# Kernel tuning notes

Measured on AMD Instinct MI355X. Metric: run time of the kernel, lower is better.

Reference implementation:

```python
import jax, jax.numpy as jnp
import numpy as np

B, T, M, C, H = 2, 2048, 2048, 1024, 16
D = C // H  # head_size = 64


def setup_inputs() -> dict:
    key = jax.random.key(0)
    ks = jax.random.split(key, 8)
    s = 0.02
    return {
        "relative_positions": jax.random.normal(ks[0], (H, T, T + M), jnp.float32),
        "x": jax.random.normal(ks[1], (B, T, C), jnp.float32),
        "xl_memory": jax.random.normal(ks[2], (B, M, 2, C), jnp.float32),
        "Wq": jax.random.normal(ks[3], (C, C), jnp.float32) * s,
        "Wk": jax.random.normal(ks[4], (C, C), jnp.float32) * s,
        "Wv": jax.random.normal(ks[5], (C, C), jnp.float32) * s,
        "Wp": jax.random.normal(ks[6], (C, C), jnp.float32) * s,
        "bp": jax.random.normal(ks[7], (C,), jnp.float32) * s,
    }


def reference(relative_positions, x, xl_memory, Wq, Wk, Wv, Wp, bp):
    b, t, c = x.shape
    h, d = H, D
    q = x @ Wq  # [b,t,c]
    k = x @ Wk
    v = x @ Wv
    k_xl = xl_memory[..., 0, :]  # [b,m,c]
    v_xl = xl_memory[..., 1, :]
    k = jnp.concatenate([k_xl, k], axis=-2)  # [b,t+m,c]
    v = jnp.concatenate([v_xl, v], axis=-2)
    tk = k.shape[1]

    def split_heads(z):  # [b,s,(h d)] -> [b,h,s,d]
        return z.reshape(z.shape[0], z.shape[1], h, d).transpose(0, 2, 1, 3)

    qh, kh, vh = split_heads(q), split_heads(k), split_heads(v)
    w = jnp.einsum("bhid,bhjd->bhij", qh, kh)  # [b,h,t,tk]
    i, j = w.shape[-2], w.shape[-1]
    # bias added BEFORE scaling, as in the original
    w = (w + relative_positions[..., -i:, -j:]) * (d ** -0.5)
    # causal mask with memory offset: mask where col > row + (j - i)
    row = jnp.arange(i)[:, None]
    col = jnp.arange(j)[None, :]
    mask = col > row + (j - i)
    w = jnp.where(mask, -jnp.inf, w)
    w = jax.nn.softmax(w, axis=-1)
    wv = jnp.einsum("bhij,bhjd->bhid", w, vh)  # [b,h,t,d]
    wv = wv.transpose(0, 2, 1, 3).reshape(b, t, c)
    out = wv @ Wp + bp
    # rebuild xl memory from full-length k,v, keep last T steps
    k_flat = kh.transpose(0, 2, 1, 3).reshape(b, tk, c)
    v_flat = vh.transpose(0, 2, 1, 3).reshape(b, tk, c)
    new_xl_memory = jnp.stack([k_flat, v_flat], axis=-2)[:, -t:]  # [b,t,2,c]
    return out, new_xl_memory
```

## Files before the change

kernel.cpp:

```cpp
#include <hip/hip_runtime.h>
#include <hip/hip_bf16.h>

constexpr int NB  = 2;
constexpr int TT  = 2048;
constexpr int MEM = 2048;
constexpr int CC  = 1024;
constexpr int NH  = 16;
constexpr int HD  = 64;
constexpr int TKK = 4096;
constexpr int BT  = NB * TT;

typedef __attribute__((ext_vector_type(8))) short short8;
typedef __attribute__((ext_vector_type(4))) float floatx4;

struct __align__(8) us4 { unsigned short x, y, z, w; };

__device__ __forceinline__ unsigned short f2bf(float f) {
  union { float f; unsigned int u; } v; v.f = f;
  return (unsigned short)((v.u + 0x7fffu + ((v.u >> 16) & 1u)) >> 16);
}

__global__ __launch_bounds__(256) void prep_xl_k(const float* __restrict__ xl,
    unsigned short* __restrict__ k_ws, unsigned short* __restrict__ v_ws) {
  int idx = blockIdx.x * 256 + threadIdx.x;
  int c   = (idx & 255) << 2;
  int rem = idx >> 8;
  int m   = rem & 2047;
  int b   = rem >> 11;
  size_t src = ((size_t)(b * MEM + m)) * 2 * CC + c;
  float4 kk = *(const float4*)&xl[src];
  float4 vv = *(const float4*)&xl[src + CC];
  int h = c >> 6, d = c & 63;
  size_t dst = ((size_t)((b * NH + h) * TKK) + m) * HD + d;
  *(us4*)&k_ws[dst] = us4{f2bf(kk.x), f2bf(kk.y), f2bf(kk.z), f2bf(kk.w)};
  *(us4*)&v_ws[dst] = us4{f2bf(vv.x), f2bf(vv.y), f2bf(vv.z), f2bf(vv.w)};
}

__global__ __launch_bounds__(256) void gemm_qkv_k(
    const float* __restrict__ x, const float* __restrict__ Wq,
    const float* __restrict__ Wk, const float* __restrict__ Wv,
    unsigned short* __restrict__ q_ws, unsigned short* __restrict__ k_ws,
    unsigned short* __restrict__ v_ws, float* __restrict__ out_xl) {
  __shared__ unsigned short As[128][32];
  __shared__ unsigned short Bs[128][40];
  const int tid = threadIdx.x;
  const int m0 = blockIdx.x * 128;
  const int nb = blockIdx.y;
  const float* __restrict__ Wsrc = (nb < 8) ? Wq : ((nb < 16) ? Wk : Wv);
  const int n0 = (nb & 7) * 128;
  const int wave = tid >> 6, lane = tid & 63;
  const int mh = (wave >> 1) * 64, nh = (wave & 1) * 64;
  const int ln = lane & 15, qd = lane >> 4;
  const floatx4 fzero = {0.f, 0.f, 0.f, 0.f};

  floatx4 acc[4][4];
#pragma unroll
  for (int i = 0; i < 4; i++)
#pragma unroll
    for (int j = 0; j < 4; j++) acc[i][j] = fzero;

  for (int kt = 0; kt < CC; kt += 32) {
    __syncthreads();
#pragma unroll
    for (int i = 0; i < 4; i++) {
      int e = tid + i * 256;
      int row = e >> 3, kc = (e & 7) << 2;
      float4 a4 = *(const float4*)&x[(size_t)(m0 + row) * CC + kt + kc];
      *(us4*)&As[row][kc] = us4{f2bf(a4.x), f2bf(a4.y), f2bf(a4.z), f2bf(a4.w)};
    }
#pragma unroll
    for (int i = 0; i < 4; i++) {
      int e = tid + i * 256;
      int n = e & 127, kg = e >> 7;
      const float* p = &Wsrc[(size_t)(kt + kg * 4) * CC + n0 + n];
      float b0 = p[0], b1 = p[CC], b2 = p[2 * CC], b3 = p[3 * CC];
      *(us4*)&Bs[n][kg * 4] = us4{f2bf(b0), f2bf(b1), f2bf(b2), f2bf(b3)};
    }
    __syncthreads();
    short8 af[4], bfr[4];
#pragma unroll
    for (int mf = 0; mf < 4; mf++) af[mf]  = *(const short8*)&As[mh + mf * 16 + ln][qd * 8];
#pragma unroll
    for (int nf = 0; nf < 4; nf++) bfr[nf] = *(const short8*)&Bs[nh + nf * 16 + ln][qd * 8];
#pragma unroll
    for (int mf = 0; mf < 4; mf++)
#pragma unroll
      for (int nf = 0; nf < 4; nf++)
        acc[mf][nf] = __builtin_amdgcn_mfma_f32_16x16x32_bf16(af[mf], bfr[nf], acc[mf][nf], 0, 0, 0);
  }

  const int sel = nb >> 3;
#pragma unroll
  for (int mf = 0; mf < 4; mf++) {
#pragma unroll
    for (int nf = 0; nf < 4; nf++) {
      int gn = n0 + nh + nf * 16 + ln;
      int h = gn >> 6, d = gn & 63;
#pragma unroll
      for (int r = 0; r < 4; r++) {
        int gm = m0 + mh + mf * 16 + qd * 4 + r;
        int b = gm >> 11, t = gm & 2047;
        float val = acc[mf][nf][r];
        unsigned short bv = f2bf(val);
        if (sel == 0) {
          q_ws[((size_t)((b * NH + h) * TT) + t) * HD + d] = bv;
        } else if (sel == 1) {
          k_ws[((size_t)((b * NH + h) * TKK) + MEM + t) * HD + d] = bv;
          out_xl[(((size_t)(b * TT + t)) * 2 + 0) * CC + gn] = val;
        } else {
          v_ws[((size_t)((b * NH + h) * TKK) + MEM + t) * HD + d] = bv;
          out_xl[(((size_t)(b * TT + t)) * 2 + 1) * CC + gn] = val;
        }
      }
    }
  }
}

__global__ __launch_bounds__(256) void attn_k(
    const unsigned short* __restrict__ q_ws, const unsigned short* __restrict__ k_ws,
    const unsigned short* __restrict__ v_ws, const float* __restrict__ rel,
    unsigned short* __restrict__ wv_ws) {
  __shared__ unsigned short Ks[64][72];
  __shared__ unsigned short Vs[64][64];
  __shared__ unsigned short Ps[4][16][64];
  const int idx = blockIdx.x;
  const int qt = 31 - (idx >> 5);
  const int h  = (idx >> 1) & 15;
  const int b  = idx & 1;
  const int tid = threadIdx.x;
  const int wave = tid >> 6, lane = tid & 63;
  const int ln = lane & 15, qd = lane >> 4;
  const int q0 = qt * 64;
  const int qrow_w = q0 + wave * 16;
  const floatx4 fzero = {0.f, 0.f, 0.f, 0.f};

  short8 qf[2];
#pragma unroll
  for (int ks = 0; ks < 2; ks++)
    qf[ks] = *(const short8*)&q_ws[((size_t)((b * NH + h) * TT) + qrow_w + ln) * HD + ks * 32 + qd * 8];

  floatx4 of[4];
  float mrow[4], lrow[4];
#pragma unroll
  for (int nf = 0; nf < 4; nf++) of[nf] = fzero;
#pragma unroll
  for (int r = 0; r < 4; r++) { mrow[r] = -1e30f; lrow[r] = 0.f; }

  const int ntiles = qt + 33;
  for (int kt = 0; kt < ntiles; kt++) {
    const int kbase = kt * 64;
    __syncthreads();
    {
      const size_t rowbase = (size_t)((b * NH + h) * TKK) + kbase;
#pragma unroll
      for (int i = 0; i < 2; i++) {
        int e = tid + i * 256;
        int r = e >> 3, c0 = (e & 7) << 3;
        *(short8*)&Ks[r][c0] = *(const short8*)&k_ws[(rowbase + r) * HD + c0];
        short8 v8 = *(const short8*)&v_ws[(rowbase + r) * HD + c0];
#pragma unroll
        for (int j = 0; j < 8; j++) {
          int d = c0 + j;
          int slot = ((r >> 3) ^ (d & 7) ^ (d >> 3)) & 7;
          Vs[d][(slot << 3) | (r & 7)] = (unsigned short)v8[j];
        }
      }
    }
    __syncthreads();

    float bias[4][4];
#pragma unroll
    for (int nf = 0; nf < 4; nf++)
#pragma unroll
      for (int r = 0; r < 4; r++)
        bias[nf][r] = rel[((size_t)(h * TT) + qrow_w + qd * 4 + r) * TKK + kbase + nf * 16 + ln];

    const bool lastTile = (kt == ntiles - 1);

    floatx4 sacc[4];
#pragma unroll
    for (int nf = 0; nf < 4; nf++) sacc[nf] = fzero;
#pragma unroll
    for (int ks = 0; ks < 2; ks++)
#pragma unroll
      for (int nf = 0; nf < 4; nf++) {
        short8 kf = *(const short8*)&Ks[nf * 16 + ln][ks * 32 + qd * 8];
        sacc[nf] = __builtin_amdgcn_mfma_f32_16x16x32_bf16(qf[ks], kf, sacc[nf], 0, 0, 0);
      }

    float sv[4][4];
#pragma unroll
    for (int nf = 0; nf < 4; nf++)
#pragma unroll
      for (int r = 0; r < 4; r++)
        sv[nf][r] = (sacc[nf][r] + bias[nf][r]) * 0.125f;
    if (lastTile) {
#pragma unroll
      for (int nf = 0; nf < 4; nf++)
#pragma unroll
        for (int r = 0; r < 4; r++) {
          int kcol = kbase + nf * 16 + ln;
          int qrow = qrow_w + qd * 4 + r;
          if (kcol > qrow + MEM) sv[nf][r] = -1e30f;
        }
    }

#pragma unroll
    for (int r = 0; r < 4; r++) {
      float mx = fmaxf(fmaxf(sv[0][r], sv[1][r]), fmaxf(sv[2][r], sv[3][r]));
#pragma unroll
      for (int off = 8; off >= 1; off >>= 1)
        mx = fmaxf(mx, __shfl_xor(mx, off, 64));
      float mnew = fmaxf(mrow[r], mx);
      float alpha = __expf(mrow[r] - mnew);
      mrow[r] = mnew;
      float sum = 0.f;
#pragma unroll
      for (int nf = 0; nf < 4; nf++) {
        float p = __expf(sv[nf][r] - mnew);
        sv[nf][r] = p;
        sum += p;
      }
#pragma unroll
      for (int off = 8; off >= 1; off >>= 1)
        sum += __shfl_xor(sum, off, 64);
      lrow[r] = lrow[r] * alpha + sum;
#pragma unroll
      for (int nf = 0; nf < 4; nf++) of[nf][r] *= alpha;
    }

#pragma unroll
    for (int nf = 0; nf < 4; nf++)
#pragma unroll
      for (int r = 0; r < 4; r++) {
        int row = qd * 4 + r;
        int col = nf * 16 + ln;
        int slot = ((col >> 3) ^ (row & 7) ^ (row >> 3)) & 7;
        Ps[wave][row][(slot << 3) | (col & 7)] = f2bf(sv[nf][r]);
      }

#pragma unroll
    for (int ks = 0; ks < 2; ks++) {
      int g = qd + 4 * ks;
      int pslot = (g ^ (ln & 7) ^ (ln >> 3)) & 7;
      short8 pf = *(const short8*)&Ps[wave][ln][pslot << 3];
#pragma unroll
      for (int nf = 0; nf < 4; nf++) {
        int dd = nf * 16 + ln;
        int vslot = (g ^ (dd & 7) ^ (dd >> 3)) & 7;
        short8 vf = *(const short8*)&Vs[dd][vslot << 3];
        of[nf] = __builtin_amdgcn_mfma_f32_16x16x32_bf16(pf, vf, of[nf], 0, 0, 0);
      }
    }
  }

  {
    float inv[4];
#pragma unroll
    for (int r = 0; r < 4; r++) inv[r] = 1.f / lrow[r];
#pragma unroll
    for (int nf = 0; nf < 4; nf++)
#pragma unroll
      for (int r = 0; r < 4; r++)
        wv_ws[((size_t)(b * TT) + qrow_w + qd * 4 + r) * CC + h * 64 + nf * 16 + ln] =
            f2bf(of[nf][r] * inv[r]);
  }
}

__global__ __launch_bounds__(256) void gemm_out_k(
    const unsigned short* __restrict__ a_bf, const float* __restrict__ Wp,
    const float* __restrict__ bp, float* __restrict__ out) {
  __shared__ unsigned short As[128][32];
  __shared__ unsigned short Bs[128][40];
  const int tid = threadIdx.x;
  const int m0 = blockIdx.x * 128;
  const int n0 = blockIdx.y * 128;
  const int wave = tid >> 6, lane = tid & 63;
  const int mh = (wave >> 1) * 64, nh = (wave & 1) * 64;
  const int ln = lane & 15, qd = lane >> 4;
  const floatx4 fzero = {0.f, 0.f, 0.f, 0.f};

  floatx4 acc[4][4];
#pragma unroll
  for (int i = 0; i < 4; i++)
#pragma unroll
    for (int j = 0; j < 4; j++) acc[i][j] = fzero;

  for (int kt = 0; kt < CC; kt += 32) {
    __syncthreads();
#pragma unroll
    for (int i = 0; i < 2; i++) {
      int e = tid + i * 256;
      int row = e >> 2, c0 = (e & 3) << 3;
      *(short8*)&As[row][c0] = *(const short8*)&a_bf[(size_t)(m0 + row) * CC + kt + c0];
    }
#pragma unroll
    for (int i = 0; i < 4; i++) {
      int e = tid + i * 256;
      int n = e & 127, kg = e >> 7;
      const float* p = &Wp[(size_t)(kt + kg * 4) * CC + n0 + n];
      float b0 = p[0], b1 = p[CC], b2 = p[2 * CC], b3 = p[3 * CC];
      *(us4*)&Bs[n][kg * 4] = us4{f2bf(b0), f2bf(b1), f2bf(b2), f2bf(b3)};
    }
    __syncthreads();
    short8 af[4], bfr[4];
#pragma unroll
    for (int mf = 0; mf < 4; mf++) af[mf]  = *(const short8*)&As[mh + mf * 16 + ln][qd * 8];
#pragma unroll
    for (int nf = 0; nf < 4; nf++) bfr[nf] = *(const short8*)&Bs[nh + nf * 16 + ln][qd * 8];
#pragma unroll
    for (int mf = 0; mf < 4; mf++)
#pragma unroll
      for (int nf = 0; nf < 4; nf++)
        acc[mf][nf] = __builtin_amdgcn_mfma_f32_16x16x32_bf16(af[mf], bfr[nf], acc[mf][nf], 0, 0, 0);
  }

#pragma unroll
  for (int mf = 0; mf < 4; mf++)
#pragma unroll
    for (int nf = 0; nf < 4; nf++) {
      int gn = n0 + nh + nf * 16 + ln;
      float bias = bp[gn];
#pragma unroll
      for (int r = 0; r < 4; r++) {
        int gm = m0 + mh + mf * 16 + qd * 4 + r;
        out[(size_t)gm * CC + gn] = acc[mf][nf][r] + bias;
      }
    }
}

extern "C" void kernel_launch(void* const* d_in, const int* in_sizes, int n_in,
                              void* d_out, int out_size, void* d_ws, size_t ws_size,
                              hipStream_t stream) {
  const float* rel = (const float*)d_in[0];
  const float* x   = (const float*)d_in[1];
  const float* xl  = (const float*)d_in[2];
  const float* Wq  = (const float*)d_in[3];
  const float* Wk  = (const float*)d_in[4];
  const float* Wv  = (const float*)d_in[5];
  const float* Wp  = (const float*)d_in[6];
  const float* bp  = (const float*)d_in[7];
  float* out    = (float*)d_out;
  float* out_xl = out + (size_t)BT * CC;

  char* ws = (char*)d_ws;
  unsigned short* q_ws  = (unsigned short*)(ws);
  unsigned short* k_ws  = (unsigned short*)(ws + (size_t)(8)  * 1024 * 1024);
  unsigned short* v_ws  = (unsigned short*)(ws + (size_t)(24) * 1024 * 1024);
  unsigned short* wv_ws = (unsigned short*)(ws + (size_t)(40) * 1024 * 1024);

  prep_xl_k<<<dim3(4096), dim3(256), 0, stream>>>(xl, k_ws, v_ws);
  gemm_qkv_k<<<dim3(32, 24), dim3(256), 0, stream>>>(x, Wq, Wk, Wv, q_ws, k_ws, v_ws, out_xl);
  attn_k<<<dim3(1024), dim3(256), 0, stream>>>(q_ws, k_ws, v_ws, rel, wv_ws);
  gemm_out_k<<<dim3(32, 8), dim3(256), 0, stream>>>(wv_ws, Wp, bp, out);
}
```

Baseline: 1.002 ms.

## Double-buffer K/V tiles and prefetch bias into registers in attention loop

The attention kernel now holds two LDS buffers for K and V. Each iteration issues the global loads for the next tile's K, V and relative-position bias into registers before doing the current tile's MFMA and softmax work, then writes them to the alternate buffer. This cuts one barrier per iteration and overlaps global memory latency with compute. V is now gathered column-wise, so each thread owns one head dim, and written with vectorized LDS stores instead of scalar scattered stores. The cost is extra registers for the prefetched data, which may lower occupancy, plus more shared memory.

```diff
diff --git a/kernel.cpp b/kernel.cpp
--- a/kernel.cpp
+++ b/kernel.cpp
@@ -120,9 +120,9 @@
     const unsigned short* __restrict__ q_ws, const unsigned short* __restrict__ k_ws,
     const unsigned short* __restrict__ v_ws, const float* __restrict__ rel,
     unsigned short* __restrict__ wv_ws) {
-  __shared__ unsigned short Ks[64][72];
-  __shared__ unsigned short Vs[64][64];
-  __shared__ unsigned short Ps[4][16][64];
+  __shared__ unsigned short Ks[2][64][72];
+  __shared__ unsigned short Vs[2][64][72];
+  __shared__ unsigned short Ps[4][16][72];
   const int idx = blockIdx.x;
   const int qt = 31 - (idx >> 5);
   const int h  = (idx >> 1) & 15;
@@ -134,11 +134,22 @@
   const int qrow_w = q0 + wave * 16;
   const floatx4 fzero = {0.f, 0.f, 0.f, 0.f};
 
+  const int kr0 = tid >> 3;
+  const int kc0 = (tid & 7) << 3;
+  const int vd  = tid & 63;
+  const int vkg = tid >> 6;
+  const size_t khbase = (size_t)((b * NH + h) * TKK);
+
   short8 qf[2];
 #pragma unroll
   for (int ks = 0; ks < 2; ks++)
     qf[ks] = *(const short8*)&q_ws[((size_t)((b * NH + h) * TT) + qrow_w + ln) * HD + ks * 32 + qd * 8];
 
+  const float* biasrow[4];
+#pragma unroll
+  for (int r = 0; r < 4; r++)
+    biasrow[r] = &rel[((size_t)(h * TT) + qrow_w + qd * 4 + r) * TKK + ln];
+
   floatx4 of[4];
   float mrow[4], lrow[4];
 #pragma unroll
@@ -147,54 +158,82 @@
   for (int r = 0; r < 4; r++) { mrow[r] = -1e30f; lrow[r] = 0.f; }
 
   const int ntiles = qt + 33;
+
+  float bcur[16];
+  {
+    short8 k0 = *(const short8*)&k_ws[(khbase + kr0) * HD + kc0];
+    short8 k1 = *(const short8*)&k_ws[(khbase + kr0 + 32) * HD + kc0];
+    ushort2 vv[8];
+    const unsigned short* vp = &v_ws[(khbase + vkg * 16) * HD + vd];
+#pragma unroll
+    for (int j = 0; j < 8; j++) {
+      vv[j].x = vp[(2 * j) * HD];
+      vv[j].y = vp[(2 * j + 1) * HD];
+    }
+#pragma unroll
+    for (int nf = 0; nf < 4; nf++)
+#pragma unroll
+      for (int r = 0; r < 4; r++)
+        bcur[nf * 4 + r] = biasrow[r][nf * 16];
+    *(short8*)&Ks[0][kr0][kc0] = k0;
+    *(short8*)&Ks[0][kr0 + 32][kc0] = k1;
+#pragma unroll
+    for (int jj = 0; jj < 2; jj++) {
+      int slot = ((vkg * 2 + jj) ^ (vd & 7) ^ (vd >> 3)) & 7;
+      short8 w;
+#pragma unroll
+      for (int t = 0; t < 4; t++) {
+        w[2 * t]     = (short)vv[jj * 4 + t].x;
+        w[2 * t + 1] = (short)vv[jj * 4 + t].y;
+      }
+      *(short8*)&Vs[0][vd][slot << 3] = w;
+    }
+  }
+  __syncthreads();
+
+  int c = 0;
   for (int kt = 0; kt < ntiles; kt++) {
     const int kbase = kt * 64;
-    __syncthreads();
-    {
-      const size_t rowbase = (size_t)((b * NH + h) * TKK) + kbase;
-#pragma unroll
-      for (int i = 0; i < 2; i++) {
-        int e = tid + i * 256;
-        int r = e >> 3, c0 = (e & 7) << 3;
-        *(short8*)&Ks[r][c0] = *(const short8*)&k_ws[(rowbase + r) * HD + c0];
-        short8 v8 = *(const short8*)&v_ws[(rowbase + r) * HD + c0];
-#pragma unroll
-        for (int j = 0; j < 8; j++) {
-          int d = c0 + j;
-          int slot = ((r >> 3) ^ (d & 7) ^ (d >> 3)) & 7;
-          Vs[d][(slot << 3) | (r & 7)] = (unsigned short)v8[j];
-        }
-      }
-    }
-    __syncthreads();
-
-    float bias[4][4];
+    const bool more = (kt + 1 < ntiles);
+
+    short8 nk0, nk1;
+    ushort2 nvv[8];
+    float bnx[16];
+    if (more) {
+      const size_t rb = khbase + kbase + 64;
+      nk0 = *(const short8*)&k_ws[(rb + kr0) * HD + kc0];
+      nk1 = *(const short8*)&k_ws[(rb + kr0 + 32) * HD + kc0];
+      const unsigned short* vp = &v_ws[(rb + vkg * 16) * HD + vd];
+#pragma unroll
+      for (int j = 0; j < 8; j++) {
+        nvv[j].x = vp[(2 * j) * HD];
+        nvv[j].y = vp[(2 * j + 1) * HD];
+      }
+#pragma unroll
+      for (int nf = 0; nf < 4; nf++)
+#pragma unroll
+        for (int r = 0; r < 4; r++)
+          bnx[nf * 4 + r] = biasrow[r][kbase + 64 + nf * 16];
+    }
+
+    floatx4 sacc[4];
+#pragma unroll
+    for (int nf = 0; nf < 4; nf++) sacc[nf] = fzero;
+#pragma unroll
+    for (int ks = 0; ks < 2; ks++)
+#pragma unroll
+      for (int nf = 0; nf < 4; nf++) {
+        short8 kf = *(const short8*)&Ks[c][nf * 16 + ln][ks * 32 + qd * 8];
+        sacc[nf] = __builtin_amdgcn_mfma_f32_16x16x32_bf16(qf[ks], kf, sacc[nf], 0, 0, 0);
+      }
+
+    float sv[4][4];
 #pragma unroll
     for (int nf = 0; nf < 4; nf++)
 #pragma unroll
       for (int r = 0; r < 4; r++)
-        bias[nf][r] = rel[((size_t)(h * TT) + qrow_w + qd * 4 + r) * TKK + kbase + nf * 16 + ln];
-
-    const bool lastTile = (kt == ntiles - 1);
-
-    floatx4 sacc[4];
-#pragma unroll
-    for (int nf = 0; nf < 4; nf++) sacc[nf] = fzero;
-#pragma unroll
-    for (int ks = 0; ks < 2; ks++)
-#pragma unroll
-      for (int nf = 0; nf < 4; nf++) {
-        short8 kf = *(const short8*)&Ks[nf * 16 + ln][ks * 32 + qd * 8];
-        sacc[nf] = __builtin_amdgcn_mfma_f32_16x16x32_bf16(qf[ks], kf, sacc[nf], 0, 0, 0);
-      }
-
-    float sv[4][4];
-#pragma unroll
-    for (int nf = 0; nf < 4; nf++)
-#pragma unroll
-      for (int r = 0; r < 4; r++)
-        sv[nf][r] = (sacc[nf][r] + bias[nf][r]) * 0.125f;
-    if (lastTile) {
+        sv[nf][r] = (sacc[nf][r] + bcur[nf * 4 + r]) * 0.125f;
+    if (kt == ntiles - 1) {
 #pragma unroll
       for (int nf = 0; nf < 4; nf++)
 #pragma unroll
@@ -248,10 +287,30 @@
       for (int nf = 0; nf < 4; nf++) {
         int dd = nf * 16 + ln;
         int vslot = (g ^ (dd & 7) ^ (dd >> 3)) & 7;
-        short8 vf = *(const short8*)&Vs[dd][vslot << 3];
+        short8 vf = *(const short8*)&Vs[c][dd][vslot << 3];
         of[nf] = __builtin_amdgcn_mfma_f32_16x16x32_bf16(pf, vf, of[nf], 0, 0, 0);
       }
     }
+
+    if (more) {
+      *(short8*)&Ks[c ^ 1][kr0][kc0] = nk0;
+      *(short8*)&Ks[c ^ 1][kr0 + 32][kc0] = nk1;
+#pragma unroll
+      for (int jj = 0; jj < 2; jj++) {
+        int slot = ((vkg * 2 + jj) ^ (vd & 7) ^ (vd >> 3)) & 7;
+        short8 w;
+#pragma unroll
+        for (int t = 0; t < 4; t++) {
+          w[2 * t]     = (short)nvv[jj * 4 + t].x;
+          w[2 * t + 1] = (short)nvv[jj * 4 + t].y;
+        }
+        *(short8*)&Vs[c ^ 1][vd][slot << 3] = w;
+      }
+#pragma unroll
+      for (int i = 0; i < 16; i++) bcur[i] = bnx[i];
+    }
+    __syncthreads();
+    c ^= 1;
   }
 
   {
```

New measurement: 992.5 us. Within noise of the previous version (-1.0%).
